# Optimization experiments

Measured on AMD Instinct MI355X. Metric: run time of the kernel, lower is better.

Reference implementation:

```python
import jax, jax.numpy as jnp
import numpy as np

B, M, F_N, D, GS, L = 32, 512, 64, 128, 4, 8  # batch, max atoms, in feats, int_d, graph channels, layers


def setup_inputs() -> dict:
    key = jax.random.key(0)
    ks = jax.random.split(key, 8)
    G = jax.random.uniform(ks[0], (B, GS, M, M), dtype=jnp.float32)      # dense multi-channel adjacency
    x = jax.random.normal(ks[1], (B, M, F_N), dtype=jnp.float32)          # per-atom features
    W0 = jax.random.normal(ks[2], (GS, F_N, D), dtype=jnp.float32) * 0.05 # per-channel Linear, layer 0
    b0 = jax.random.normal(ks[3], (GS, D), dtype=jnp.float32) * 0.05
    Wl = jax.random.normal(ks[4], (L - 1, GS, D, D), dtype=jnp.float32) * 0.05
    bl = jax.random.normal(ks[5], (L - 1, GS, D), dtype=jnp.float32) * 0.05
    Wout = jax.random.normal(ks[6], (D, 1), dtype=jnp.float32) * 0.05
    bout = jax.random.normal(ks[7], (1,), dtype=jnp.float32) * 0.05
    return {"G": G, "x": x, "W0": W0, "b0": b0, "Wl": Wl, "bl": bl, "Wout": Wout, "bout": bout}


def _graph_mat_layer(G, h, W, b):
    # per-channel linear: [B,M,C] x [GS,C,P] -> [B,GS,M,P]
    multi = jnp.einsum('bmc,gcp->bgmp', h, W) + b[None, :, None, :]
    # per-sample, per-channel adjacency matmul: [B,GS,M,M] @ [B,GS,M,P]
    xout = jnp.einsum('bgmn,bgnp->bgmp', G, multi)
    # ReLU then goodmax aggregation over graph channels (dim=1)
    return jnp.max(jax.nn.relu(xout), axis=1)  # [B,M,P]


def reference(G, x, W0, b0, Wl, bl, Wout, bout):
    # layer 0: input width F_N != D, so no residual (shape mismatch)
    h = _graph_mat_layer(G, x, W0, b0)
    # layers 1..L-1: resnet skip (shapes match)
    for i in range(L - 1):
        h = _graph_mat_layer(G, h, Wl[i], bl[i]) + h
    # lin_out on [B,M,D] -> [B,M,1]
    return h @ Wout + bout
```

## Files before the change

### kernel.cpp

```cpp
#include <hip/hip_runtime.h>
#include <stdint.h>


#define B_  32
#define M_  512
#define FN_ 64
#define D_  128
#define GS_ 4
#define L_  8

typedef __attribute__((ext_vector_type(8))) short short8;
typedef __attribute__((ext_vector_type(4))) float f32x4;
typedef unsigned short us;

__device__ __forceinline__ us f2bf(float f) {
  union { float f; unsigned int u; } v; v.f = f;
  return (us)((v.u + 0x7FFFu + ((v.u >> 16) & 1u)) >> 16);
}

__device__ __forceinline__ void gl16(const void* g, void* l) {
  __builtin_amdgcn_global_load_lds((const __attribute__((address_space(1))) void*)g,
                                   (__attribute__((address_space(3))) void*)l, 16, 0, 0);
}

__global__ void k_conv(const float4* __restrict__ src, ushort4* __restrict__ dst, int n4) {
  int i = blockIdx.x * blockDim.x + threadIdx.x;
  const int st = gridDim.x * blockDim.x;
  for (; i < n4; i += st) {
    float4 v = src[i];
    ushort4 o;
    o.x = f2bf(v.x); o.y = f2bf(v.y); o.z = f2bf(v.z); o.w = f2bf(v.w);
    dst[i] = o;
  }
}

__global__ void k_convW(const float* __restrict__ W0, const float* __restrict__ Wl,
                        us* __restrict__ W0T, us* __restrict__ WlT) {
  int i = blockIdx.x * blockDim.x + threadIdx.x;
  const int n0 = GS_ * FN_ * D_;
  if (i < n0) {
    int g = i / (FN_ * D_), r = i % (FN_ * D_), c = r / D_, p = r % D_;
    W0T[((size_t)g * D_ + p) * FN_ + c] = f2bf(W0[i]);
  } else {
    int j = i - n0;
    if (j < 7 * GS_ * D_ * D_) {
      int l = j / (GS_ * D_ * D_), r = j % (GS_ * D_ * D_);
      int g = r / (D_ * D_), r2 = r % (D_ * D_), c = r2 / D_, p = r2 % D_;
      WlT[(((size_t)l * GS_ + g) * D_ + p) * D_ + c] = f2bf(Wl[j]);
    }
  }
}

template<int NKA, int CC>
__device__ __forceinline__ void stageA(const us* __restrict__ Wt,
                                       const float* __restrict__ bias,
                                       us* __restrict__ Mw,
                                       const us* hbL, us (*smS)[24576],
                                       int g, int hf, int lr, int kq,
                                       int srow, int scol, int kk, int b, int mt) {
  f32x4 acc[4][4];
#pragma unroll
  for (int i = 0; i < 4; ++i)
#pragma unroll
    for (int j = 0; j < 4; ++j) acc[i][j] = (f32x4){0.f, 0.f, 0.f, 0.f};

#define STGA(bufi, ks) do { \
    us* bb_ = smS[bufi] + g * 6144; \
    _Pragma("unroll") \
    for (int u_ = 0; u_ < 4; ++u_) { \
      const us* sp_ = Wt + (size_t)g * D_ * CC + (size_t)(hf * 64 + u_ * 16 + srow) * CC \
                      + (ks) * 32 + scol; \
      gl16(sp_, bb_ + 2048 + (hf * 4 + u_) * 512); \
    } \
  } while (0)

  STGA(0, 0);
  STGA(1, 1);
  const int cm = (CC == 64) ? 7 : 15;
#pragma unroll
  for (int ks = 0; ks < NKA; ++ks) {
    if (ks < NKA - 1) asm volatile("s_waitcnt vmcnt(4)" ::: "memory");
    else              asm volatile("s_waitcnt vmcnt(0)" ::: "memory");
    __builtin_amdgcn_sched_barrier(0);
    const us* sb = smS[ks % 3] + g * 6144 + 2048;
    short8 af[4], bf[4];
#pragma unroll
    for (int i = 0; i < 4; ++i)
      af[i] = *(const short8*)&hbL[(i * 16 + lr) * 128 + (((ks * 4 + kq) ^ (lr & cm)) << 3)];
#pragma unroll
    for (int j = 0; j < 4; ++j)
      bf[j] = *(const short8*)&sb[(hf * 64 + j * 16 + lr) * 32 + kk];
    if (ks + 2 < NKA) STGA((ks + 2) % 3, ks + 2);
    asm volatile("s_waitcnt lgkmcnt(0)" ::: "memory");
    __builtin_amdgcn_sched_barrier(0);
#pragma unroll
    for (int i = 0; i < 4; ++i)
#pragma unroll
      for (int j = 0; j < 4; ++j)
        acc[i][j] = __builtin_amdgcn_mfma_f32_16x16x32_bf16(af[i], bf[j], acc[i][j], 0, 0, 0);
  }
#undef STGA

#pragma unroll
  for (int j = 0; j < 4; ++j) {
    const int p = hf * 64 + j * 16 + lr;
    const float bv = bias[g * D_ + p];
    us* op = Mw + ((size_t)(b * GS_ + g) * D_ + p) * M_;
#pragma unroll
    for (int i = 0; i < 4; ++i) {
      const int n0 = mt * 64 + i * 16 + kq * 4;
      f32x4 v = acc[i][j];
      ushort4 o;
      o.x = f2bf(v[0] + bv); o.y = f2bf(v[1] + bv);
      o.z = f2bf(v[2] + bv); o.w = f2bf(v[3] + bv);
      *(ushort4*)(op + n0) = o;
    }
  }
}

__launch_bounds__(512, 1)
__global__ void k_pre(const float* __restrict__ x,
                      const us* __restrict__ W0T, const float* __restrict__ b0,
                      us* __restrict__ Mh0) {
  __shared__ __align__(16) us smS[2][24576];
  __shared__ __align__(16) us hbL[8192];

  const int bid = blockIdx.x;
  const int swz = (bid & 7) * 32 + (bid >> 3);
  const int b = swz >> 3, mt = swz & 7;

  const int t = threadIdx.x;
  const int w = t >> 6, g = w >> 1, hf = w & 1;
  const int lane = t & 63, lr = lane & 15, kq = lane >> 4;
  const int srow = lane >> 2;
  const int scol = ((lane & 3) ^ ((lane >> 3) & 3)) * 8;
  const int kk = (kq ^ ((lr >> 1) & 3)) * 8;

  {
    const int row = t >> 3, c8 = t & 7;
    const float* xs = x + ((size_t)b * M_ + mt * 64 + row) * FN_ + c8 * 8;
    float4 v0 = *(const float4*)xs, v1 = *(const float4*)(xs + 4);
    ushort4 o0, o1;
    o0.x = f2bf(v0.x); o0.y = f2bf(v0.y); o0.z = f2bf(v0.z); o0.w = f2bf(v0.w);
    o1.x = f2bf(v1.x); o1.y = f2bf(v1.y); o1.z = f2bf(v1.z); o1.w = f2bf(v1.w);
    us* dp = hbL + row * 128 + ((c8 ^ (row & 7)) << 3);
    *(ushort4*)dp = o0; *(ushort4*)(dp + 4) = o1;
  }
  __syncthreads();

  stageA<FN_ / 32, FN_>(W0T, b0, Mh0, hbL, smS, g, hf, lr, kq, srow, scol, kk, b, mt);
}

template<int FIRST, int LAST>
__launch_bounds__(512, 1)
__global__ void k_fused(const us* __restrict__ Gh, const us* __restrict__ Min,
                        us* __restrict__ Mout,
                        const us* __restrict__ WT, const float* __restrict__ bias,
                        float* __restrict__ h,
                        const float* __restrict__ Wout, const float* __restrict__ bout,
                        float* __restrict__ out) {
  __shared__ __align__(16) us smS[3][24576];
  __shared__ __align__(16) us hbL[8192];

  const int bid = blockIdx.x;
  const int swz = (bid & 7) * 32 + (bid >> 3);
  const int b = swz >> 3, mt = swz & 7;

  const int t = threadIdx.x;
  const int w = t >> 6, g = w >> 1, hf = w & 1;
  const int lane = t & 63, lr = lane & 15, kq = lane >> 4;
  const int srow = lane >> 2;
  const int scol = ((lane & 3) ^ ((lane >> 3) & 3)) * 8;
  const int kk = (kq ^ ((lr >> 1) & 3)) * 8;
  const int m_l = t >> 3, pq = t & 7;

  const us* AgB = Gh + ((size_t)(b * GS_ + g) * M_ + mt * 64) * M_;
  const us* BgB = Min + (size_t)(b * GS_ + g) * D_ * M_;
  f32x4 acc[4][4];
#pragma unroll
  for (int i = 0; i < 4; ++i)
#pragma unroll
    for (int j = 0; j < 4; ++j) acc[i][j] = (f32x4){0.f, 0.f, 0.f, 0.f};

#define STGB(bufi, ks) do { \
    us* bb_ = smS[bufi] + g * 6144; \
    _Pragma("unroll") \
    for (int u_ = 0; u_ < 6; ++u_) { \
      const int ls_ = hf * 6 + u_; \
      const us* sp_ = (ls_ < 4) \
        ? AgB + (size_t)(ls_ * 16 + srow) * M_ + (ks) * 32 + scol \
        : BgB + (size_t)((ls_ - 4) * 16 + srow) * M_ + (ks) * 32 + scol; \
      gl16(sp_, bb_ + ls_ * 512 + lane * 8); \
    } \
  } while (0)

  STGB(0, 0);
  STGB(1, 1);
#pragma unroll
  for (int ks = 0; ks < 16; ++ks) {
    if (ks < 15) asm volatile("s_waitcnt vmcnt(6)" ::: "memory");
    else         asm volatile("s_waitcnt vmcnt(0)" ::: "memory");
    __builtin_amdgcn_s_barrier();
    __builtin_amdgcn_sched_barrier(0);
    const us* sa = smS[ks % 3] + g * 6144;
    const us* sb = sa + 2048;
    short8 af[4], bf[4];
#pragma unroll
    for (int i = 0; i < 4; ++i)
      af[i] = *(const short8*)&sa[(i * 16 + lr) * 32 + kk];
#pragma unroll
    for (int j = 0; j < 4; ++j)
      bf[j] = *(const short8*)&sb[(hf * 64 + j * 16 + lr) * 32 + kk];
    if (ks + 2 < 16) STGB((ks + 2) % 3, ks + 2);
    asm volatile("s_waitcnt lgkmcnt(0)" ::: "memory");
    __builtin_amdgcn_sched_barrier(0);
#pragma unroll
    for (int i = 0; i < 4; ++i)
#pragma unroll
      for (int j = 0; j < 4; ++j)
        acc[i][j] = __builtin_amdgcn_mfma_f32_16x16x32_bf16(af[i], bf[j], acc[i][j], 0, 0, 0);
  }
#undef STGB

  __builtin_amdgcn_s_barrier();
  __builtin_amdgcn_sched_barrier(0);

  {
    float* red = (float*)smS + (size_t)g * 8192;
#pragma unroll
    for (int i = 0; i < 4; ++i)
#pragma unroll
      for (int j = 0; j < 4; ++j) {
        const int col = hf * 64 + j * 16 + lr;
        const int ch = col >> 2, cw = col & 3;
#pragma unroll
        for (int cc = 0; cc < 4; ++cc) {
          const int row = i * 16 + kq * 4 + cc;
          red[row * 128 + ((ch ^ (row & 7)) << 2) + cw] = fmaxf(acc[i][j][cc], 0.f);
        }
      }
  }
  __builtin_amdgcn_s_barrier();
  __builtin_amdgcn_sched_barrier(0);

  f32x4 hreg[4];
  {
    const float* red = (const float*)smS;
#pragma unroll
    for (int k = 0; k < 4; ++k) {
      const int ch = pq * 4 + k;
      const float* rp = red + (size_t)m_l * 128 + ((ch ^ (m_l & 7)) << 2);
      f32x4 v = *(const f32x4*)rp;
#pragma unroll
      for (int gg = 1; gg < 4; ++gg) {
        f32x4 u = *(const f32x4*)(rp + (size_t)gg * 8192);
        v[0] = fmaxf(v[0], u[0]); v[1] = fmaxf(v[1], u[1]);
        v[2] = fmaxf(v[2], u[2]); v[3] = fmaxf(v[3], u[3]);
      }
      hreg[k] = v;
    }
  }
  const size_t ho = ((size_t)b * M_ + mt * 64 + m_l) * D_ + pq * 16;
  float4* hp = (float4*)(h + ho);
  if (!FIRST) {
#pragma unroll
    for (int k = 0; k < 4; ++k) {
      float4 hv = hp[k];
      hreg[k][0] += hv.x; hreg[k][1] += hv.y; hreg[k][2] += hv.z; hreg[k][3] += hv.w;
    }
  }

  if constexpr (!LAST) {
#pragma unroll
    for (int k = 0; k < 4; ++k)
      hp[k] = (float4){hreg[k][0], hreg[k][1], hreg[k][2], hreg[k][3]};
    us* d0 = hbL + m_l * 128 + (((2 * pq) ^ (m_l & 15)) << 3);
    us* d1 = hbL + m_l * 128 + (((2 * pq + 1) ^ (m_l & 15)) << 3);
    ushort4 o0, o1, o2, o3;
    o0.x = f2bf(hreg[0][0]); o0.y = f2bf(hreg[0][1]); o0.z = f2bf(hreg[0][2]); o0.w = f2bf(hreg[0][3]);
    o1.x = f2bf(hreg[1][0]); o1.y = f2bf(hreg[1][1]); o1.z = f2bf(hreg[1][2]); o1.w = f2bf(hreg[1][3]);
    o2.x = f2bf(hreg[2][0]); o2.y = f2bf(hreg[2][1]); o2.z = f2bf(hreg[2][2]); o2.w = f2bf(hreg[2][3]);
    o3.x = f2bf(hreg[3][0]); o3.y = f2bf(hreg[3][1]); o3.z = f2bf(hreg[3][2]); o3.w = f2bf(hreg[3][3]);
    *(ushort4*)d0 = o0; *(ushort4*)(d0 + 4) = o1;
    *(ushort4*)d1 = o2; *(ushort4*)(d1 + 4) = o3;
    __syncthreads();

    stageA<D_ / 32, D_>(WT, bias, Mout, hbL, smS, g, hf, lr, kq, srow, scol, kk, b, mt);
  } else {
    float s = 0.f;
#pragma unroll
    for (int k = 0; k < 4; ++k) {
      const float4 wv = *(const float4*)(Wout + pq * 16 + k * 4);
      s += hreg[k][0] * wv.x + hreg[k][1] * wv.y + hreg[k][2] * wv.z + hreg[k][3] * wv.w;
    }
    s += __shfl_xor(s, 1);
    s += __shfl_xor(s, 2);
    s += __shfl_xor(s, 4);
    if (pq == 0) out[(size_t)b * M_ + mt * 64 + m_l] = s + bout[0];
  }
}

extern "C" void kernel_launch(void* const* d_in, const int* in_sizes, int n_in,
                              void* d_out, int out_size, void* d_ws, size_t ws_size,
                              hipStream_t stream) {
  const float* G    = (const float*)d_in[0];
  const float* x    = (const float*)d_in[1];
  const float* W0   = (const float*)d_in[2];
  const float* b0   = (const float*)d_in[3];
  const float* Wl   = (const float*)d_in[4];
  const float* bl   = (const float*)d_in[5];
  const float* Wout = (const float*)d_in[6];
  const float* bout = (const float*)d_in[7];

  char* ws = (char*)d_ws;
  us*   Gh  = (us*)(ws);
  us*   Mh0 = (us*)(ws + 67108864);
  us*   Mh1 = (us*)(ws + 83886080);
  float* h  = (float*)(ws + 100663296);
  us*   W0T = (us*)(ws + 109051904);
  us*   WlT = (us*)(ws + 109051904 + 65536);
  float* out = (float*)d_out;

  k_convW<<<1920, 256, 0, stream>>>(W0, Wl, W0T, WlT);
  k_conv<<<2048, 256, 0, stream>>>((const float4*)G, (ushort4*)Gh, (B_ * GS_ * M_ * M_) / 4);
  k_pre<<<256, 512, 0, stream>>>(x, W0T, b0, Mh0);

  k_fused<1, 0><<<256, 512, 0, stream>>>(Gh, Mh0, Mh1,
      WlT + (size_t)0 * GS_ * D_ * D_, bl + (size_t)0 * GS_ * D_,
      h, Wout, bout, out);
  for (int l = 1; l < L_ - 1; ++l) {
    const us* Min = (l & 1) ? Mh1 : Mh0;
    us* Mout      = (l & 1) ? Mh0 : Mh1;
    k_fused<0, 0><<<256, 512, 0, stream>>>(Gh, Min, Mout,
        WlT + (size_t)l * GS_ * D_ * D_, bl + (size_t)l * GS_ * D_,
        h, Wout, bout, out);
  }
  k_fused<0, 1><<<256, 512, 0, stream>>>(Gh, (L_ - 1) & 1 ? Mh1 : Mh0, nullptr,
      nullptr, nullptr, h, Wout, bout, out);
}
```

Baseline: 274.3 us.

## Fuse G fp32-to-bf16 conversion into first graph layer kernel

Removes the standalone pass that converts G to bf16. The first fused layer kernel now reads fp32 G directly, converts it in registers with packed bf16 conversion instructions, feeds it to the MFMAs, and writes the bf16 copy out for the later layers. This saves one full read of G plus a kernel launch, at the cost of heavier global loads and register pressure in the first layer's main loop.

After: 274.1 us. Within noise of the previous version (-0.1%).

```diff
diff --git a/kernel.cpp b/kernel.cpp
--- a/kernel.cpp
+++ b/kernel.cpp
@@ -18,20 +18,18 @@
   return (us)((v.u + 0x7FFFu + ((v.u >> 16) & 1u)) >> 16);
 }
 
+__device__ __forceinline__ short8 cvt8(float4 a, float4 b) {
+  union { unsigned int u[4]; short8 s; } r;
+  asm("v_cvt_pk_bf16_f32 %0, %1, %2" : "=v"(r.u[0]) : "v"(a.x), "v"(a.y));
+  asm("v_cvt_pk_bf16_f32 %0, %1, %2" : "=v"(r.u[1]) : "v"(a.z), "v"(a.w));
+  asm("v_cvt_pk_bf16_f32 %0, %1, %2" : "=v"(r.u[2]) : "v"(b.x), "v"(b.y));
+  asm("v_cvt_pk_bf16_f32 %0, %1, %2" : "=v"(r.u[3]) : "v"(b.z), "v"(b.w));
+  return r.s;
+}
+
 __device__ __forceinline__ void gl16(const void* g, void* l) {
   __builtin_amdgcn_global_load_lds((const __attribute__((address_space(1))) void*)g,
                                    (__attribute__((address_space(3))) void*)l, 16, 0, 0);
-}
-
-__global__ void k_conv(const float4* __restrict__ src, ushort4* __restrict__ dst, int n4) {
-  int i = blockIdx.x * blockDim.x + threadIdx.x;
-  const int st = gridDim.x * blockDim.x;
-  for (; i < n4; i += st) {
-    float4 v = src[i];
-    ushort4 o;
-    o.x = f2bf(v.x); o.y = f2bf(v.y); o.z = f2bf(v.z); o.w = f2bf(v.w);
-    dst[i] = o;
-  }
 }
 
 __global__ void k_convW(const float* __restrict__ W0, const float* __restrict__ Wl,
@@ -151,6 +149,149 @@
   stageA<FN_ / 32, FN_>(W0T, b0, Mh0, hbL, smS, g, hf, lr, kq, srow, scol, kk, b, mt);
 }
 
+__launch_bounds__(512, 1)
+__global__ void k_fusedC(const float* __restrict__ G, const us* __restrict__ Min,
+                         us* __restrict__ Mout, us* __restrict__ Gh,
+                         const us* __restrict__ WT, const float* __restrict__ bias,
+                         float* __restrict__ h) {
+  __shared__ __align__(16) us smS[3][24576];
+  __shared__ __align__(16) us hbL[8192];
+
+  const int bid = blockIdx.x;
+  const int swz = (bid & 7) * 32 + (bid >> 3);
+  const int b = swz >> 3, mt = swz & 7;
+
+  const int t = threadIdx.x;
+  const int w = t >> 6, g = w >> 1, hf = w & 1;
+  const int lane = t & 63, lr = lane & 15, kq = lane >> 4;
+  const int srow = lane >> 2;
+  const int scol = ((lane & 3) ^ ((lane >> 3) & 3)) * 8;
+  const int kk = (kq ^ ((lr >> 1) & 3)) * 8;
+  const int m_l = t >> 3, pq = t & 7;
+
+  const float* Ag = G + ((size_t)(b * GS_ + g) * M_ + mt * 64) * M_;
+  us* Ghp = Gh + ((size_t)(b * GS_ + g) * M_ + mt * 64) * M_;
+  const us* BgB = Min + (size_t)(b * GS_ + g) * D_ * M_;
+
+#define STGC(bufi, ks) do { \
+    us* bb_ = smS[bufi] + g * 6144; \
+    _Pragma("unroll") \
+    for (int u_ = 0; u_ < 4; ++u_) { \
+      const int ls_ = 4 + hf * 4 + u_; \
+      const us* sp_ = BgB + (size_t)((ls_ - 4) * 16 + srow) * M_ + (ks) * 32 + scol; \
+      gl16(sp_, bb_ + ls_ * 512 + lane * 8); \
+    } \
+  } while (0)
+
+#define LDA(AR, ks) do { \
+    _Pragma("unroll") \
+    for (int i_ = 0; i_ < 4; ++i_) { \
+      const float* ap_ = Ag + (size_t)(i_ * 16 + lr) * M_ + (ks) * 32 + kq * 8; \
+      AR[2 * i_]     = *(const float4*)ap_; \
+      AR[2 * i_ + 1] = *(const float4*)(ap_ + 4); \
+    } \
+  } while (0)
+
+#define BODY(ks, AR) do { \
+    if ((ks) < 15) asm volatile("s_waitcnt vmcnt(12)" ::: "memory"); \
+    else           asm volatile("s_waitcnt vmcnt(0)" ::: "memory"); \
+    __builtin_amdgcn_sched_barrier(0); \
+    short8 af[4], bf[4]; \
+    _Pragma("unroll") \
+    for (int i_ = 0; i_ < 4; ++i_) af[i_] = cvt8(AR[2 * i_], AR[2 * i_ + 1]); \
+    if (hf == 0) { \
+      _Pragma("unroll") \
+      for (int i_ = 0; i_ < 4; ++i_) \
+        *(short8*)(Ghp + (size_t)(i_ * 16 + lr) * M_ + (ks) * 32 + kq * 8) = af[i_]; \
+    } \
+    { const us* sb_ = smS[(ks) % 3] + g * 6144 + 2048; \
+      _Pragma("unroll") \
+      for (int j_ = 0; j_ < 4; ++j_) \
+        bf[j_] = *(const short8*)&sb_[(hf * 64 + j_ * 16 + lr) * 32 + kk]; } \
+    if ((ks) + 2 < 16) { LDA(AR, (ks) + 2); STGC(((ks) + 2) % 3, (ks) + 2); } \
+    asm volatile("s_waitcnt lgkmcnt(0)" ::: "memory"); \
+    __builtin_amdgcn_sched_barrier(0); \
+    _Pragma("unroll") \
+    for (int i_ = 0; i_ < 4; ++i_) \
+      _Pragma("unroll") \
+      for (int j_ = 0; j_ < 4; ++j_) \
+        acc[i_][j_] = __builtin_amdgcn_mfma_f32_16x16x32_bf16(af[i_], bf[j_], acc[i_][j_], 0, 0, 0); \
+  } while (0)
+
+  f32x4 acc[4][4];
+#pragma unroll
+  for (int i = 0; i < 4; ++i)
+#pragma unroll
+    for (int j = 0; j < 4; ++j) acc[i][j] = (f32x4){0.f, 0.f, 0.f, 0.f};
+
+  float4 aA[8], aB[8];
+  LDA(aA, 0); STGC(0, 0);
+  LDA(aB, 1); STGC(1, 1);
+
+#pragma unroll
+  for (int kp = 0; kp < 8; ++kp) {
+    BODY(2 * kp, aA);
+    BODY(2 * kp + 1, aB);
+  }
+#undef BODY
+#undef LDA
+#undef STGC
+
+  __syncthreads();
+
+  {
+    float* red = (float*)smS + (size_t)g * 8192;
+#pragma unroll
+    for (int i = 0; i < 4; ++i)
+#pragma unroll
+      for (int j = 0; j < 4; ++j) {
+        const int col = hf * 64 + j * 16 + lr;
+        const int ch = col >> 2, cw = col & 3;
+#pragma unroll
+        for (int cc = 0; cc < 4; ++cc) {
+          const int row = i * 16 + kq * 4 + cc;
+          red[row * 128 + ((ch ^ (row & 7)) << 2) + cw] = fmaxf(acc[i][j][cc], 0.f);
+        }
+      }
+  }
+  __syncthreads();
+
+  f32x4 hreg[4];
+  {
+    const float* red = (const float*)smS;
+#pragma unroll
+    for (int k = 0; k < 4; ++k) {
+      const int ch = pq * 4 + k;
+      const float* rp = red + (size_t)m_l * 128 + ((ch ^ (m_l & 7)) << 2);
+      f32x4 v = *(const f32x4*)rp;
+#pragma unroll
+      for (int gg = 1; gg < 4; ++gg) {
+        f32x4 u = *(const f32x4*)(rp + (size_t)gg * 8192);
+        v[0] = fmaxf(v[0], u[0]); v[1] = fmaxf(v[1], u[1]);
+        v[2] = fmaxf(v[2], u[2]); v[3] = fmaxf(v[3], u[3]);
+      }
+      hreg[k] = v;
+    }
+  }
+  const size_t ho = ((size_t)b * M_ + mt * 64 + m_l) * D_ + pq * 16;
+  float4* hp = (float4*)(h + ho);
+#pragma unroll
+  for (int k = 0; k < 4; ++k)
+    hp[k] = (float4){hreg[k][0], hreg[k][1], hreg[k][2], hreg[k][3]};
+  us* d0 = hbL + m_l * 128 + (((2 * pq) ^ (m_l & 15)) << 3);
+  us* d1 = hbL + m_l * 128 + (((2 * pq + 1) ^ (m_l & 15)) << 3);
+  ushort4 o0, o1, o2, o3;
+  o0.x = f2bf(hreg[0][0]); o0.y = f2bf(hreg[0][1]); o0.z = f2bf(hreg[0][2]); o0.w = f2bf(hreg[0][3]);
+  o1.x = f2bf(hreg[1][0]); o1.y = f2bf(hreg[1][1]); o1.z = f2bf(hreg[1][2]); o1.w = f2bf(hreg[1][3]);
+  o2.x = f2bf(hreg[2][0]); o2.y = f2bf(hreg[2][1]); o2.z = f2bf(hreg[2][2]); o2.w = f2bf(hreg[2][3]);
+  o3.x = f2bf(hreg[3][0]); o3.y = f2bf(hreg[3][1]); o3.z = f2bf(hreg[3][2]); o3.w = f2bf(hreg[3][3]);
+  *(ushort4*)d0 = o0; *(ushort4*)(d0 + 4) = o1;
+  *(ushort4*)d1 = o2; *(ushort4*)(d1 + 4) = o3;
+  __syncthreads();
+
+  stageA<D_ / 32, D_>(WT, bias, Mout, hbL, (us (*)[24576])smS, g, hf, lr, kq, srow, scol, kk, b, mt);
+}
+
 template<int FIRST, int LAST>
 __launch_bounds__(512, 1)
 __global__ void k_fused(const us* __restrict__ Gh, const us* __restrict__ Min,
@@ -322,12 +463,11 @@
   float* out = (float*)d_out;
 
   k_convW<<<1920, 256, 0, stream>>>(W0, Wl, W0T, WlT);
-  k_conv<<<2048, 256, 0, stream>>>((const float4*)G, (ushort4*)Gh, (B_ * GS_ * M_ * M_) / 4);
   k_pre<<<256, 512, 0, stream>>>(x, W0T, b0, Mh0);
 
-  k_fused<1, 0><<<256, 512, 0, stream>>>(Gh, Mh0, Mh1,
-      WlT + (size_t)0 * GS_ * D_ * D_, bl + (size_t)0 * GS_ * D_,
-      h, Wout, bout, out);
+  k_fusedC<<<256, 512, 0, stream>>>(G, Mh0, Mh1,
+      Gh, WlT + (size_t)0 * GS_ * D_ * D_, bl + (size_t)0 * GS_ * D_, h);
+
   for (int l = 1; l < L_ - 1; ++l) {
     const us* Min = (l & 1) ? Mh1 : Mh0;
     us* Mout      = (l & 1) ? Mh0 : Mh1;
```

## Halve row tile to 32, load B/weights directly to registers, raise occupancy

Applied to the files above, without the earlier changes.

Each block now covers 32 atom rows instead of 64, so the grid doubles to 512 blocks and launch bounds allow up to 4 blocks per CU. The Min (B) operand and the weight operand are read from global memory straight into registers with double buffering, and only the G tile is staged in LDS, which cuts shared memory to about 40KB. The channel-max reduction is done in two passes over column halves so the smaller LDS buffer suffices. This aims to fill 256 CUs and hide latency through occupancy, at the cost of redundant global reads of B across the two row halves and uncoalesced per-lane register loads.

New measurement: 422.0 us. 1.54x slower.

```diff
diff --git a/kernel.cpp b/kernel.cpp
--- a/kernel.cpp
+++ b/kernel.cpp
@@ -54,52 +54,38 @@
 template<int NKA, int CC>
 __device__ __forceinline__ void stageA(const us* __restrict__ Wt,
                                        const float* __restrict__ bias,
-                                       us* __restrict__ Mw,
-                                       const us* hbL, us (*smS)[24576],
-                                       int g, int hf, int lr, int kq,
-                                       int srow, int scol, int kk, int b, int mt) {
-  f32x4 acc[4][4];
-#pragma unroll
-  for (int i = 0; i < 4; ++i)
+                                       us* __restrict__ Mw, const us* hbL,
+                                       int g, int hf, int lr, int kq, int b, int mt) {
+  const int cm = (CC == 64) ? 7 : 15;
+  const us* Wg = Wt + (size_t)g * D_ * CC + (size_t)(hf * 64) * CC;
+  f32x4 acc[2][4];
+#pragma unroll
+  for (int i = 0; i < 2; ++i)
 #pragma unroll
     for (int j = 0; j < 4; ++j) acc[i][j] = (f32x4){0.f, 0.f, 0.f, 0.f};
 
-#define STGA(bufi, ks) do { \
-    us* bb_ = smS[bufi] + g * 6144; \
-    _Pragma("unroll") \
-    for (int u_ = 0; u_ < 4; ++u_) { \
-      const us* sp_ = Wt + (size_t)g * D_ * CC + (size_t)(hf * 64 + u_ * 16 + srow) * CC \
-                      + (ks) * 32 + scol; \
-      gl16(sp_, bb_ + 2048 + (hf * 4 + u_) * 512); \
-    } \
+#define LDW(WR, ks) do { _Pragma("unroll") \
+    for (int j_ = 0; j_ < 4; ++j_) \
+      WR[j_] = *(const short8*)(Wg + (size_t)(j_ * 16 + lr) * CC + (ks) * 32 + kq * 8); \
   } while (0)
 
-  STGA(0, 0);
-  STGA(1, 1);
-  const int cm = (CC == 64) ? 7 : 15;
+  short8 wA[4], wB[4];
+  LDW(wA, 0);
 #pragma unroll
   for (int ks = 0; ks < NKA; ++ks) {
-    if (ks < NKA - 1) asm volatile("s_waitcnt vmcnt(4)" ::: "memory");
-    else              asm volatile("s_waitcnt vmcnt(0)" ::: "memory");
-    __builtin_amdgcn_sched_barrier(0);
-    const us* sb = smS[ks % 3] + g * 6144 + 2048;
-    short8 af[4], bf[4];
-#pragma unroll
-    for (int i = 0; i < 4; ++i)
+    if (ks + 1 < NKA) { if (ks & 1) LDW(wA, ks + 1); else LDW(wB, ks + 1); }
+    short8 af[2];
+#pragma unroll
+    for (int i = 0; i < 2; ++i)
       af[i] = *(const short8*)&hbL[(i * 16 + lr) * 128 + (((ks * 4 + kq) ^ (lr & cm)) << 3)];
-#pragma unroll
-    for (int j = 0; j < 4; ++j)
-      bf[j] = *(const short8*)&sb[(hf * 64 + j * 16 + lr) * 32 + kk];
-    if (ks + 2 < NKA) STGA((ks + 2) % 3, ks + 2);
-    asm volatile("s_waitcnt lgkmcnt(0)" ::: "memory");
-    __builtin_amdgcn_sched_barrier(0);
-#pragma unroll
-    for (int i = 0; i < 4; ++i)
+    const short8* wf = (ks & 1) ? wB : wA;
+#pragma unroll
+    for (int i = 0; i < 2; ++i)
 #pragma unroll
       for (int j = 0; j < 4; ++j)
-        acc[i][j] = __builtin_amdgcn_mfma_f32_16x16x32_bf16(af[i], bf[j], acc[i][j], 0, 0, 0);
-  }
-#undef STGA
+        acc[i][j] = __builtin_amdgcn_mfma_f32_16x16x32_bf16(af[i], wf[j], acc[i][j], 0, 0, 0);
+  }
+#undef LDW
 
 #pragma unroll
   for (int j = 0; j < 4; ++j) {
@@ -107,8 +93,8 @@
     const float bv = bias[g * D_ + p];
     us* op = Mw + ((size_t)(b * GS_ + g) * D_ + p) * M_;
 #pragma unroll
-    for (int i = 0; i < 4; ++i) {
-      const int n0 = mt * 64 + i * 16 + kq * 4;
+    for (int i = 0; i < 2; ++i) {
+      const int n0 = mt * 32 + i * 16 + kq * 4;
       f32x4 v = acc[i][j];
       ushort4 o;
       o.x = f2bf(v[0] + bv); o.y = f2bf(v[1] + bv);
@@ -118,16 +104,48 @@
   }
 }
 
-__launch_bounds__(512, 1)
-__global__ void k_pre(const float* __restrict__ x,
-                      const us* __restrict__ W0T, const float* __restrict__ b0,
-                      us* __restrict__ Mh0) {
-  __shared__ __align__(16) us smS[2][24576];
-  __shared__ __align__(16) us hbL[8192];
-
+__launch_bounds__(512, 4)
+__global__ void k_pre(const float* __restrict__ x, const us* __restrict__ W0T,
+                      const float* __restrict__ b0, us* __restrict__ Mh0) {
+  __shared__ __align__(16) us hbL[4096];
   const int bid = blockIdx.x;
-  const int swz = (bid & 7) * 32 + (bid >> 3);
-  const int b = swz >> 3, mt = swz & 7;
+  const int swz = (bid & 7) * 64 + (bid >> 3);
+  const int b = swz >> 4, mt = swz & 15;
+  const int t = threadIdx.x;
+  const int w = t >> 6, g = w >> 1, hf = w & 1;
+  const int lane = t & 63, lr = lane & 15, kq = lane >> 4;
+  {
+    const int row = t >> 4, c8 = t & 15;
+    if (c8 < 8) {
+      const float* xs = x + ((size_t)b * M_ + mt * 32 + row) * FN_ + c8 * 8;
+      float4 v0 = *(const float4*)xs, v1 = *(const float4*)(xs + 4);
+      ushort4 o0, o1;
+      o0.x = f2bf(v0.x); o0.y = f2bf(v0.y); o0.z = f2bf(v0.z); o0.w = f2bf(v0.w);
+      o1.x = f2bf(v1.x); o1.y = f2bf(v1.y); o1.z = f2bf(v1.z); o1.w = f2bf(v1.w);
+      us* dp = hbL + row * 128 + ((c8 ^ (row & 7)) << 3);
+      *(ushort4*)dp = o0; *(ushort4*)(dp + 4) = o1;
+    }
+  }
+  __syncthreads();
+  stageA<FN_ / 32, FN_>(W0T, b0, Mh0, hbL, g, hf, lr, kq, b, mt);
+}
+
+template<int FIRST, int LAST>
+__launch_bounds__(512, 4)
+__global__ void k_fused(const us* __restrict__ Gh, const us* __restrict__ Min,
+                        us* __restrict__ Mout,
+                        const us* __restrict__ WT, const float* __restrict__ bias,
+                        float* __restrict__ h,
+                        const float* __restrict__ Wout, const float* __restrict__ bout,
+                        float* __restrict__ out) {
+  __shared__ __align__(16) us sm[20480];
+  us* Ast = sm;
+  float* red = (float*)sm;
+  us* hbL = sm + 16384;
+
+  const int bid = blockIdx.x;
+  const int swz = (bid & 7) * 64 + (bid >> 3);
+  const int b = swz >> 4, mt = swz & 15;
 
   const int t = threadIdx.x;
   const int w = t >> 6, g = w >> 1, hf = w & 1;
@@ -136,167 +154,111 @@
   const int scol = ((lane & 3) ^ ((lane >> 3) & 3)) * 8;
   const int kk = (kq ^ ((lr >> 1) & 3)) * 8;
 
-  {
-    const int row = t >> 3, c8 = t & 7;
-    const float* xs = x + ((size_t)b * M_ + mt * 64 + row) * FN_ + c8 * 8;
-    float4 v0 = *(const float4*)xs, v1 = *(const float4*)(xs + 4);
-    ushort4 o0, o1;
-    o0.x = f2bf(v0.x); o0.y = f2bf(v0.y); o0.z = f2bf(v0.z); o0.w = f2bf(v0.w);
-    o1.x = f2bf(v1.x); o1.y = f2bf(v1.y); o1.z = f2bf(v1.z); o1.w = f2bf(v1.w);
-    us* dp = hbL + row * 128 + ((c8 ^ (row & 7)) << 3);
-    *(ushort4*)dp = o0; *(ushort4*)(dp + 4) = o1;
-  }
-  __syncthreads();
-
-  stageA<FN_ / 32, FN_>(W0T, b0, Mh0, hbL, smS, g, hf, lr, kq, srow, scol, kk, b, mt);
-}
-
-template<int FIRST, int LAST>
-__launch_bounds__(512, 1)
-__global__ void k_fused(const us* __restrict__ Gh, const us* __restrict__ Min,
-                        us* __restrict__ Mout,
-                        const us* __restrict__ WT, const float* __restrict__ bias,
-                        float* __restrict__ h,
-                        const float* __restrict__ Wout, const float* __restrict__ bout,
-                        float* __restrict__ out) {
-  __shared__ __align__(16) us smS[3][24576];
-  __shared__ __align__(16) us hbL[8192];
-
-  const int bid = blockIdx.x;
-  const int swz = (bid & 7) * 32 + (bid >> 3);
-  const int b = swz >> 3, mt = swz & 7;
-
-  const int t = threadIdx.x;
-  const int w = t >> 6, g = w >> 1, hf = w & 1;
-  const int lane = t & 63, lr = lane & 15, kq = lane >> 4;
-  const int srow = lane >> 2;
-  const int scol = ((lane & 3) ^ ((lane >> 3) & 3)) * 8;
-  const int kk = (kq ^ ((lr >> 1) & 3)) * 8;
-  const int m_l = t >> 3, pq = t & 7;
-
-  const us* AgB = Gh + ((size_t)(b * GS_ + g) * M_ + mt * 64) * M_;
-  const us* BgB = Min + (size_t)(b * GS_ + g) * D_ * M_;
-  f32x4 acc[4][4];
-#pragma unroll
-  for (int i = 0; i < 4; ++i)
+  const us* AgB = Gh + ((size_t)(b * GS_ + g) * M_ + mt * 32) * M_;
+  const us* Bg  = Min + (size_t)(b * GS_ + g) * D_ * M_;
+
+#define STA(bufi, ks) \
+    gl16(AgB + (size_t)(hf * 16 + srow) * M_ + (ks) * 32 + scol, \
+         Ast + (bufi) * 4096 + g * 1024 + hf * 512 + lane * 8)
+
+#define LDB(BR, ks) do { _Pragma("unroll") \
+    for (int j_ = 0; j_ < 4; ++j_) \
+      BR[j_] = *(const short8*)(Bg + (size_t)(hf * 64 + j_ * 16 + lr) * M_ + (ks) * 32 + kq * 8); \
+  } while (0)
+
+  f32x4 acc[2][4];
+#pragma unroll
+  for (int i = 0; i < 2; ++i)
 #pragma unroll
     for (int j = 0; j < 4; ++j) acc[i][j] = (f32x4){0.f, 0.f, 0.f, 0.f};
 
-#define STGB(bufi, ks) do { \
-    us* bb_ = smS[bufi] + g * 6144; \
-    _Pragma("unroll") \
-    for (int u_ = 0; u_ < 6; ++u_) { \
-      const int ls_ = hf * 6 + u_; \
-      const us* sp_ = (ls_ < 4) \
-        ? AgB + (size_t)(ls_ * 16 + srow) * M_ + (ks) * 32 + scol \
-        : BgB + (size_t)((ls_ - 4) * 16 + srow) * M_ + (ks) * 32 + scol; \
-      gl16(sp_, bb_ + ls_ * 512 + lane * 8); \
-    } \
-  } while (0)
-
-  STGB(0, 0);
-  STGB(1, 1);
+  short8 bfA[4], bfB[4];
+  STA(0, 0); STA(1, 1); LDB(bfA, 0);
+
 #pragma unroll
   for (int ks = 0; ks < 16; ++ks) {
-    if (ks < 15) asm volatile("s_waitcnt vmcnt(6)" ::: "memory");
-    else         asm volatile("s_waitcnt vmcnt(0)" ::: "memory");
+    if (ks == 0)      asm volatile("s_waitcnt vmcnt(5)" ::: "memory");
+    else if (ks < 15) asm volatile("s_waitcnt vmcnt(9)" ::: "memory");
+    else              asm volatile("s_waitcnt vmcnt(8)" ::: "memory");
     __builtin_amdgcn_s_barrier();
     __builtin_amdgcn_sched_barrier(0);
-    const us* sa = smS[ks % 3] + g * 6144;
-    const us* sb = sa + 2048;
-    short8 af[4], bf[4];
-#pragma unroll
-    for (int i = 0; i < 4; ++i)
-      af[i] = *(const short8*)&sa[(i * 16 + lr) * 32 + kk];
-#pragma unroll
-    for (int j = 0; j < 4; ++j)
-      bf[j] = *(const short8*)&sb[(hf * 64 + j * 16 + lr) * 32 + kk];
-    if (ks + 2 < 16) STGB((ks + 2) % 3, ks + 2);
+    const us* sa = Ast + (ks % 3) * 4096 + g * 1024;
+    short8 af[2];
+#pragma unroll
+    for (int i = 0; i < 2; ++i)
+      af[i] = *(const short8*)&sa[i * 512 + lr * 32 + kk];
+    if (ks + 2 < 16) STA((ks + 2) % 3, ks + 2);
+    if (ks + 1 < 16) { if (ks & 1) LDB(bfA, ks + 1); else LDB(bfB, ks + 1); }
     asm volatile("s_waitcnt lgkmcnt(0)" ::: "memory");
     __builtin_amdgcn_sched_barrier(0);
-#pragma unroll
-    for (int i = 0; i < 4; ++i)
+    const short8* bf = (ks & 1) ? bfB : bfA;
+#pragma unroll
+    for (int i = 0; i < 2; ++i)
 #pragma unroll
       for (int j = 0; j < 4; ++j)
         acc[i][j] = __builtin_amdgcn_mfma_f32_16x16x32_bf16(af[i], bf[j], acc[i][j], 0, 0, 0);
   }
-#undef STGB
-
-  __builtin_amdgcn_s_barrier();
-  __builtin_amdgcn_sched_barrier(0);
-
-  {
-    float* red = (float*)smS + (size_t)g * 8192;
-#pragma unroll
-    for (int i = 0; i < 4; ++i)
-#pragma unroll
-      for (int j = 0; j < 4; ++j) {
-        const int col = hf * 64 + j * 16 + lr;
-        const int ch = col >> 2, cw = col & 3;
-#pragma unroll
-        for (int cc = 0; cc < 4; ++cc) {
-          const int row = i * 16 + kq * 4 + cc;
-          red[row * 128 + ((ch ^ (row & 7)) << 2) + cw] = fmaxf(acc[i][j][cc], 0.f);
+#undef STA
+#undef LDB
+
+  float sdot = 0.f;
+  const int row_r = t >> 4;
+  const int c4 = t & 15;
+#pragma unroll
+  for (int p = 0; p < 2; ++p) {
+    __builtin_amdgcn_s_barrier();
+    if (hf == p) {
+#pragma unroll
+      for (int i = 0; i < 2; ++i)
+#pragma unroll
+        for (int j = 0; j < 4; ++j) {
+          const int colL = j * 16 + lr;
+          const int ch = colL >> 2, cw = colL & 3;
+#pragma unroll
+          for (int cc = 0; cc < 4; ++cc) {
+            const int row = i * 16 + kq * 4 + cc;
+            red[g * 2048 + row * 64 + ((ch ^ (row & 15)) << 2) + cw] =
+                fmaxf(acc[i][j][cc], 0.f);
+          }
         }
-      }
-  }
-  __builtin_amdgcn_s_barrier();
-  __builtin_amdgcn_sched_barrier(0);
-
-  f32x4 hreg[4];
-  {
-    const float* red = (const float*)smS;
-#pragma unroll
-    for (int k = 0; k < 4; ++k) {
-      const int ch = pq * 4 + k;
-      const float* rp = red + (size_t)m_l * 128 + ((ch ^ (m_l & 7)) << 2);
-      f32x4 v = *(const f32x4*)rp;
-#pragma unroll
-      for (int gg = 1; gg < 4; ++gg) {
-        f32x4 u = *(const f32x4*)(rp + (size_t)gg * 8192);
-        v[0] = fmaxf(v[0], u[0]); v[1] = fmaxf(v[1], u[1]);
-        v[2] = fmaxf(v[2], u[2]); v[3] = fmaxf(v[3], u[3]);
-      }
-      hreg[k] = v;
-    }
-  }
-  const size_t ho = ((size_t)b * M_ + mt * 64 + m_l) * D_ + pq * 16;
-  float4* hp = (float4*)(h + ho);
-  if (!FIRST) {
-#pragma unroll
-    for (int k = 0; k < 4; ++k) {
-      float4 hv = hp[k];
-      hreg[k][0] += hv.x; hreg[k][1] += hv.y; hreg[k][2] += hv.z; hreg[k][3] += hv.w;
+    }
+    __builtin_amdgcn_s_barrier();
+    const int cs = (c4 ^ (row_r & 15)) << 2;
+    const float* rp = red + row_r * 64 + cs;
+    f32x4 v = *(const f32x4*)rp;
+#pragma unroll
+    for (int gg = 1; gg < 4; ++gg) {
+      f32x4 u = *(const f32x4*)(rp + gg * 2048);
+      v[0] = fmaxf(v[0], u[0]); v[1] = fmaxf(v[1], u[1]);
+      v[2] = fmaxf(v[2], u[2]); v[3] = fmaxf(v[3], u[3]);
+    }
+    const size_t ho = ((size_t)b * M_ + mt * 32 + row_r) * D_ + p * 64 + c4 * 4;
+    float4* hp = (float4*)(h + ho);
+    if (!FIRST) {
+      float4 hv = *hp;
+      v[0] += hv.x; v[1] += hv.y; v[2] += hv.z; v[3] += hv.w;
+    }
+    if constexpr (!LAST) {
+      *hp = (float4){v[0], v[1], v[2], v[3]};
+      ushort4 o;
+      o.x = f2bf(v[0]); o.y = f2bf(v[1]); o.z = f2bf(v[2]); o.w = f2bf(v[3]);
+      us* dp = hbL + row_r * 128 + ((((c4 >> 1) + 8 * p) ^ (row_r & 15)) << 3) + (c4 & 1) * 4;
+      *(ushort4*)dp = o;
+    } else {
+      const float4 wv = *(const float4*)(Wout + p * 64 + c4 * 4);
+      sdot += v[0] * wv.x + v[1] * wv.y + v[2] * wv.z + v[3] * wv.w;
     }
   }
 
   if constexpr (!LAST) {
-#pragma unroll
-    for (int k = 0; k < 4; ++k)
-      hp[k] = (float4){hreg[k][0], hreg[k][1], hreg[k][2], hreg[k][3]};
-    us* d0 = hbL + m_l * 128 + (((2 * pq) ^ (m_l & 15)) << 3);
-    us* d1 = hbL + m_l * 128 + (((2 * pq + 1) ^ (m_l & 15)) << 3);
-    ushort4 o0, o1, o2, o3;
-    o0.x = f2bf(hreg[0][0]); o0.y = f2bf(hreg[0][1]); o0.z = f2bf(hreg[0][2]); o0.w = f2bf(hreg[0][3]);
-    o1.x = f2bf(hreg[1][0]); o1.y = f2bf(hreg[1][1]); o1.z = f2bf(hreg[1][2]); o1.w = f2bf(hreg[1][3]);
-    o2.x = f2bf(hreg[2][0]); o2.y = f2bf(hreg[2][1]); o2.z = f2bf(hreg[2][2]); o2.w = f2bf(hreg[2][3]);
-    o3.x = f2bf(hreg[3][0]); o3.y = f2bf(hreg[3][1]); o3.z = f2bf(hreg[3][2]); o3.w = f2bf(hreg[3][3]);
-    *(ushort4*)d0 = o0; *(ushort4*)(d0 + 4) = o1;
-    *(ushort4*)d1 = o2; *(ushort4*)(d1 + 4) = o3;
-    __syncthreads();
-
-    stageA<D_ / 32, D_>(WT, bias, Mout, hbL, smS, g, hf, lr, kq, srow, scol, kk, b, mt);
+    __builtin_amdgcn_s_barrier();
+    stageA<D_ / 32, D_>(WT, bias, Mout, hbL, g, hf, lr, kq, b, mt);
   } else {
-    float s = 0.f;
-#pragma unroll
-    for (int k = 0; k < 4; ++k) {
-      const float4 wv = *(const float4*)(Wout + pq * 16 + k * 4);
-      s += hreg[k][0] * wv.x + hreg[k][1] * wv.y + hreg[k][2] * wv.z + hreg[k][3] * wv.w;
-    }
-    s += __shfl_xor(s, 1);
-    s += __shfl_xor(s, 2);
-    s += __shfl_xor(s, 4);
-    if (pq == 0) out[(size_t)b * M_ + mt * 64 + m_l] = s + bout[0];
+    sdot += __shfl_xor(sdot, 1);
+    sdot += __shfl_xor(sdot, 2);
+    sdot += __shfl_xor(sdot, 4);
+    sdot += __shfl_xor(sdot, 8);
+    if ((t & 15) == 0) out[(size_t)b * M_ + mt * 32 + row_r] = sdot + bout[0];
   }
 }
 
@@ -323,18 +285,18 @@
 
   k_convW<<<1920, 256, 0, stream>>>(W0, Wl, W0T, WlT);
   k_conv<<<2048, 256, 0, stream>>>((const float4*)G, (ushort4*)Gh, (B_ * GS_ * M_ * M_) / 4);
-  k_pre<<<256, 512, 0, stream>>>(x, W0T, b0, Mh0);
-
-  k_fused<1, 0><<<256, 512, 0, stream>>>(Gh, Mh0, Mh1,
+  k_pre<<<512, 512, 0, stream>>>(x, W0T, b0, Mh0);
+
+  k_fused<1, 0><<<512, 512, 0, stream>>>(Gh, Mh0, Mh1,
       WlT + (size_t)0 * GS_ * D_ * D_, bl + (size_t)0 * GS_ * D_,
       h, Wout, bout, out);
   for (int l = 1; l < L_ - 1; ++l) {
     const us* Min = (l & 1) ? Mh1 : Mh0;
     us* Mout      = (l & 1) ? Mh0 : Mh1;
-    k_fused<0, 0><<<256, 512, 0, stream>>>(Gh, Min, Mout,
+    k_fused<0, 0><<<512, 512, 0, stream>>>(Gh, Min, Mout,
         WlT + (size_t)l * GS_ * D_ * D_, bl + (size_t)l * GS_ * D_,
         h, Wout, bout, out);
   }
-  k_fused<0, 1><<<256, 512, 0, stream>>>(Gh, (L_ - 1) & 1 ? Mh1 : Mh0, nullptr,
+  k_fused<0, 1><<<512, 512, 0, stream>>>(Gh, (L_ - 1) & 1 ? Mh1 : Mh0, nullptr,
       nullptr, nullptr, h, Wout, bout, out);
 }
```
